# Performance work log

Hardware: AMD Instinct MI355X
Metric: run time of the kernel (lower is better)

## Reference

```python
import jax, jax.numpy as jnp
import numpy as np

NUM_PERSISTENT = 16
ALIBI_ALPHA = 1.0
START_I = 0
DILATION = 1
LN_EPS = 1e-5


def setup_inputs() -> dict:
    key = jax.random.key(0)
    ks = jax.random.split(key, 16)
    B, S, C, H = 8, 1024, 512, 8
    D = C // H
    P = NUM_PERSISTENT
    Kk = 3
    x = jax.random.normal(ks[0], (B, S, C), dtype=jnp.float32)
    mask = jnp.ones((B, 1, S, S), dtype=jnp.int32)
    sc = 0.02
    Wq = jax.random.normal(ks[1], (D, D), jnp.float32) * sc
    Wk = jax.random.normal(ks[2], (D, D), jnp.float32) * sc
    Wv = jax.random.normal(ks[3], (D, D), jnp.float32) * sc
    pk = jax.random.normal(ks[4], (P, H, D), jnp.float32) * sc
    pv = jax.random.normal(ks[5], (P, H, D), jnp.float32) * sc
    th_pre = jax.random.normal(ks[6], (H, H), jnp.float32) * (1.0 / np.sqrt(H))
    th_post = jax.random.normal(ks[7], (H, H), jnp.float32) * (1.0 / np.sqrt(H))
    fc_w = jax.random.normal(ks[8], (C, C), jnp.float32) * sc
    fc_b = jnp.zeros((C,), jnp.float32)
    conv1_w = jax.random.normal(ks[9], (C, C, Kk), jnp.float32) * 0.01
    conv1_b = jnp.zeros((C,), jnp.float32)
    conv2_w = jax.random.normal(ks[10], (C, C, Kk), jnp.float32) * 0.01
    conv2_b = jnp.zeros((C,), jnp.float32)
    ln_g = jnp.ones((C,), jnp.float32)
    ln_b = jnp.zeros((C,), jnp.float32)
    return dict(x=x, mask=mask, Wq=Wq, Wk=Wk, Wv=Wv, pk=pk, pv=pv,
                th_pre=th_pre, th_post=th_post, fc_w=fc_w, fc_b=fc_b,
                conv1_w=conv1_w, conv1_b=conv1_b, conv2_w=conv2_w,
                conv2_b=conv2_b, ln_g=ln_g, ln_b=ln_b)


def _causal_conv(x_nct, w_oik, b_o, dilation):
    # padding (k-1)*d on both sides + chomp right == pad left only
    k = w_oik.shape[-1]
    p = (k - 1) * dilation
    y = jax.lax.conv_general_dilated(
        x_nct, w_oik, window_strides=(1,), padding=[(p, 0)],
        rhs_dilation=(dilation,), dimension_numbers=("NCH", "OIH", "NCH"))
    return y + b_o[None, :, None]


def reference(x, mask, Wq, Wk, Wv, pk, pv, th_pre, th_post, fc_w, fc_b,
              conv1_w, conv1_b, conv2_w, conv2_b, ln_g, ln_b):
    N, S, C = x.shape
    H = th_pre.shape[0]
    D = C // H
    P = pk.shape[0]

    # ---- MultiHeadAttention (eval: dropout = identity) ----
    xh = x.reshape(N, S, H, D)
    q = jnp.einsum("nshd,ed->nshe", xh, Wq)
    k = jnp.einsum("nshd,ed->nshe", xh, Wk)
    v = jnp.einsum("nshd,ed->nshe", xh, Wv)
    # persistent memory tokens appended along key/value length
    k = jnp.concatenate([k, jnp.broadcast_to(pk[None], (N, P, H, D))], axis=1)
    v = jnp.concatenate([v, jnp.broadcast_to(pv[None], (N, P, H, D))], axis=1)

    energy = jnp.einsum("nqhd,nkhd->nhqk", q, k)  # (N,H,S,S+P)

    # ALiBi bias (symmetric |q-k|), zero over persistent keys
    slopes = 2.0 ** (-(ALIBI_ALPHA * (jnp.arange(1, H + 1, dtype=jnp.float32) + START_I)))
    t = jnp.arange(S, dtype=jnp.float32)
    dist = jnp.abs(t[:, None] - t[None, :])  # (S,S)
    bias = -dist[None, None] * slopes[None, :, None, None]  # (1,H,S,S)
    bias = jnp.pad(bias, ((0, 0), (0, 0), (0, 0), (0, P)))
    energy = energy + bias

    # pre-softmax talking heads (1x1 conv over head axis)
    energy = jnp.einsum("hg,ngqk->nhqk", th_pre, energy)

    ext_mask = jnp.pad(mask, ((0, 0), (0, 0), (0, 0), (0, P)), constant_values=1)
    energy = jnp.where(ext_mask == 0, jnp.float32(-1e4), energy)

    attn = jax.nn.softmax(energy / jnp.sqrt(jnp.float32(C)), axis=-1)
    attn = jnp.einsum("hg,ngqk->nhqk", th_post, attn)

    att_out = jnp.einsum("nhql,nlhd->nqhd", attn, v).reshape(N, S, C)
    att_out = att_out @ fc_w.T + fc_b

    x = x + att_out  # residual (dropout1 identity in eval)

    # ---- TemporalBlock (causal dilated convs, no SE since heads>0) ----
    xc = jnp.transpose(x, (0, 2, 1))  # (N,C,S)
    h = jax.nn.relu(_causal_conv(xc, conv1_w, conv1_b, DILATION))
    h = jax.nn.relu(_causal_conv(h, conv2_w, conv2_b, DILATION))
    out = jax.nn.relu(h + xc)  # downsample is None (in==out)

    # mask out invalid frames
    conv_mask = mask[:, 0, :, 0][:, None, :]  # (N,1,S)
    out = jnp.where(conv_mask == 0, 0.0, out)

    y = jnp.transpose(out, (0, 2, 1))  # (N,S,C)
    mu = jnp.mean(y, axis=-1, keepdims=True)
    var = jnp.mean(jnp.square(y - mu), axis=-1, keepdims=True)
    y = (y - mu) * jax.lax.rsqrt(var + LN_EPS) * ln_g + ln_b
    return y
```

## Files before the change

### kernel.cpp

```cpp
#include <hip/hip_runtime.h>
#include <hip/hip_bf16.h>

#define BN 8
#define SS 1024
#define CC 512
#define HH 8
#define DD 64
#define PP 16
#define KT 1040

typedef __hip_bfloat16 bf16;
typedef unsigned char uchar;
typedef unsigned short ushort;
typedef unsigned int uint;
typedef __attribute__((ext_vector_type(8))) short short8;
typedef __attribute__((ext_vector_type(4))) float f32x4;
typedef __attribute__((ext_vector_type(2))) float f32x2;

__device__ __forceinline__ short f2s(float v){ bf16 b = __float2bfloat16(v); return *(short*)&b; }
__device__ __forceinline__ float s2f(short s){ bf16 b; *(short*)&b = s; return __bfloat162float(b); }
__device__ __forceinline__ uchar f2q(float v){
    return (uchar)__builtin_amdgcn_cvt_pk_fp8_f32(v, v, 0, false);
}

#define MFMA16(a,b,c)  __builtin_amdgcn_mfma_f32_16x16x32_bf16(a,b,c,0,0,0)
#define MFMAF8(a,b,c)  __builtin_amdgcn_mfma_f32_16x16x32_fp8_fp8(a,b,c,0,0,0)

__global__ __launch_bounds__(256) void prep_kernel(
    const float* __restrict__ fc_w, const float* __restrict__ c1w,
    const float* __restrict__ c2w, const float* __restrict__ Wq,
    const float* __restrict__ Wk, const float* __restrict__ Wv,
    const float* __restrict__ th_post,
    const float* __restrict__ pk, const float* __restrict__ pv,
    short* __restrict__ Bfc, uchar* __restrict__ Bc1,
    uchar* __restrict__ Bc2, short* __restrict__ Bqkv,
    uchar* __restrict__ kf, uchar* __restrict__ vt)
{
    int i = blockIdx.x*256 + threadIdx.x;
    const int NFC = 512*512, NCV = 512*1536, NQ = 3*64*64, NP = BN*HH*PP*DD;
    if (i < NFC) {
        int c = i >> 9, r = i & 511;
        int g = r >> 6, d = r & 63;
        float s = 0.f;
        #pragma unroll
        for (int h = 0; h < 8; ++h)
            s += fc_w[(size_t)c*512 + h*64 + d] * th_post[h*8 + g];
        Bfc[i] = f2s(s);
        return;
    }
    i -= NFC;
    if (i < NCV) {
        int o = i/1536, r = i%1536, dk = r>>9, ci = r&511;
        Bc1[i] = f2q(c1w[(o*512+ci)*3+dk] * 16.f); return;
    }
    i -= NCV;
    if (i < NCV) {
        int o = i/1536, r = i%1536, dk = r>>9, ci = r&511;
        Bc2[i] = f2q(c2w[(o*512+ci)*3+dk] * 16.f); return;
    }
    i -= NCV;
    if (i < NQ) {
        int w = i >> 12, rest = i & 4095;
        const float* W = (w==0)?Wq:(w==1)?Wk:Wv;
        Bqkv[i] = f2s(W[((rest>>6)&63)*64 + (rest&63)]);
        return;
    }
    i -= NQ;
    if (i < NP) {
        int d = i & 63, p = (i >> 6) & 15, h = (i >> 10) & 7, n = i >> 13;
        size_t src = ((size_t)p*HH + h)*DD + d;
        kf[(((size_t)(n*HH+h))*KT + SS + p)*DD + d] = f2q(pk[src]);
        vt[(((size_t)(n*HH+h))*DD + d)*KT + SS + p] = f2q(pv[src]);
    }
}

__global__ __launch_bounds__(256) void qkv_mfma(
    const float* __restrict__ x, const short* __restrict__ Bqkv,
    uchar* __restrict__ qf, uchar* __restrict__ kf, uchar* __restrict__ vt)
{
    __shared__ short Xs[64*72];
    __shared__ short Ws[192*72];
    const int tid = threadIdx.x;
    const int lin = blockIdx.x;
    const int xcd = lin & 7, slot = lin >> 3;
    const int m0 = (xcd*16 + (slot & 15))*64;
    const int h = slot >> 4;
    const int wave = tid >> 6, lane = tid & 63;
    const int lr = lane & 15, lq = lane >> 4;

    for (int i = tid; i < 1024; i += 256) {
        int r = i >> 4, cg = (i & 15)*4;
        float4 v = *(const float4*)(x + (size_t)(m0+r)*CC + h*64 + cg);
        Xs[r*72+cg+0] = f2s(v.x); Xs[r*72+cg+1] = f2s(v.y);
        Xs[r*72+cg+2] = f2s(v.z); Xs[r*72+cg+3] = f2s(v.w);
    }
    for (int i = tid; i < 3072; i += 256) {
        int r = i >> 4, cg = (i & 15)*4;
        *(short4*)(Ws + r*72 + cg) = *(const short4*)(Bqkv + (size_t)r*64 + cg);
    }
    __syncthreads();

    f32x4 acc[12];
    #pragma unroll
    for (int nt = 0; nt < 12; ++nt) acc[nt] = {0.f,0.f,0.f,0.f};
    #pragma unroll
    for (int ks = 0; ks < 2; ++ks) {
        int ko = ks*32 + lq*8;
        short8 a = *(const short8*)(Xs + (wave*16 + lr)*72 + ko);
        #pragma unroll
        for (int nt = 0; nt < 12; ++nt) {
            short8 b = *(const short8*)(Ws + (nt*16 + lr)*72 + ko);
            acc[nt] = MFMA16(a, b, acc[nt]);
        }
    }
    #pragma unroll
    for (int nt = 0; nt < 12; ++nt) {
        int ep = nt*16 + lr;
        int w = ep >> 6, e = ep & 63;
        #pragma unroll
        for (int reg = 0; reg < 4; ++reg) {
            int m = m0 + wave*16 + lq*4 + reg;
            int n = m >> 10, s = m & 1023;
            float v = acc[nt][reg];
            if (w == 0)      qf[((size_t)(n*HH+h)*SS + s)*DD + e] = f2q(v);
            else if (w == 1) kf[((size_t)(n*HH+h)*KT + s)*DD + e] = f2q(v);
            else             vt[(((size_t)(n*HH+h))*DD + e)*KT + s] = f2q(v);
        }
    }
}

__device__ __forceinline__ void en_loadK(const uchar* __restrict__ kf,
    int nh, int kt, int tid, uint2* rk)
{
    #pragma unroll
    for (int j = 0; j < 2; ++j) {
        int i = tid + j*256;
        int r = i >> 3, c8 = (i & 7)*8;
        int kcol = kt*64 + r;
        uint2 v = {0u, 0u};
        if (kcol < KT)
            v = *(const uint2*)(kf + ((size_t)nh*KT + kcol)*DD + c8);
        rk[j] = v;
    }
}

__global__ __launch_bounds__(256) void energy_mfma8(
    const uchar* __restrict__ qf, const uchar* __restrict__ kf,
    uchar* __restrict__ E)
{
    __shared__ uchar Qs[64*72];
    __shared__ uchar Ks[64*72];
    const int tid = threadIdx.x;
    const int lin = blockIdx.x + 16*blockIdx.y;
    const int xcd = lin & 7, slot = lin >> 3;
    const int nh = xcd*8 + (slot & 7);
    const int mt = slot >> 3;
    const int wave = tid >> 6, lane = tid & 63;
    const int lr = lane & 15, lq = lane >> 4;
    const int n = nh >> 3, h = nh & 7;

    #pragma unroll
    for (int j = 0; j < 2; ++j) {
        int i = tid + j*256;
        int r = i >> 3, c8 = (i & 7)*8;
        *(uint2*)(Qs + r*72 + c8) =
            *(const uint2*)(qf + ((size_t)nh*SS + mt*64 + r)*DD + c8);
    }

    uint2 rk[2];
    en_loadK(kf, nh, 0, tid, rk);

    for (int kt = 0; kt < 17; ++kt) {
        if (kt) __syncthreads();
        #pragma unroll
        for (int j = 0; j < 2; ++j) {
            int i = tid + j*256;
            *(uint2*)(Ks + (i >> 3)*72 + (i & 7)*8) = rk[j];
        }
        __syncthreads();
        if (kt + 1 < 17) en_loadK(kf, nh, kt+1, tid, rk);

        f32x4 acc[4];
        #pragma unroll
        for (int nt = 0; nt < 4; ++nt) acc[nt] = {0.f,0.f,0.f,0.f};
        #pragma unroll
        for (int ks = 0; ks < 2; ++ks) {
            int ko = ks*32 + lq*8;
            long a = *(const long*)(Qs + (wave*16 + lr)*72 + ko);
            #pragma unroll
            for (int nt = 0; nt < 4; ++nt) {
                long b = *(const long*)(Ks + (nt*16 + lr)*72 + ko);
                acc[nt] = MFMAF8(a, b, acc[nt]);
            }
        }
        #pragma unroll
        for (int nt = 0; nt < 4; ++nt) {
            int kcol = kt*64 + nt*16 + lr;
            if (kcol >= KT) continue;
            #pragma unroll
            for (int reg = 0; reg < 4; ++reg) {
                int q = mt*64 + wave*16 + lq*4 + reg;
                E[(((size_t)(n*SS + q))*HH + h)*KT + kcol] = f2q(acc[nt][reg]);
            }
        }
    }
}

__global__ __launch_bounds__(256) void softmax_kernel(
    uchar* __restrict__ E, const int* __restrict__ mask,
    const float* __restrict__ th_pre)
{
    __shared__ float thp[64];
    __shared__ float wred[4][8];
    const int tid = threadIdx.x;
    const int wave = tid >> 6, lane = tid & 63;
    const int blk = blockIdx.x;
    const int n = blk >> 10, q = blk & 1023;
    const float invs = 0.044194173824159216f;
    const float l2e  = 1.4426950408889634f;
    if (tid < 64) thp[tid] = th_pre[tid]*(invs*l2e);
    __syncthreads();
    uchar* Eb = E + (size_t)blk*HH*KT;

    const float sl[8] = {0.5f,0.25f,0.125f,0.0625f,
                         0.03125f,0.015625f,0.0078125f,0.00390625f};
    const int* mrow = mask + (size_t)n*SS*SS + (size_t)q*SS;

    const int k0 = tid*4;
    const int4 mk = *(const int4*)(mrow + k0);
    f32x4 dist;
    dist.x = fabsf((float)(q - k0));
    dist.y = fabsf((float)(q - k0 - 1));
    dist.z = fabsf((float)(q - k0 - 2));
    dist.w = fabsf((float)(q - k0 - 3));

    f32x4 tp[8];
    float tl[8];
    float sm[8];
    #pragma unroll
    for (int g = 0; g < 8; ++g) { sm[g] = 0.f; tl[g] = 0.f; }

    {
        f32x4 a[8];
        #pragma unroll
        for (int g = 0; g < 8; ++g) {
            uint u = *(const uint*)(Eb + g*KT + k0);
            f32x2 lo = __builtin_amdgcn_cvt_pk_f32_fp8((int)u, false);
            f32x2 hi = __builtin_amdgcn_cvt_pk_f32_fp8((int)u, true);
            f32x4 r; r.x = lo.x; r.y = lo.y; r.z = hi.x; r.w = hi.y;
            a[g] = r - dist*sl[g];
        }
        #pragma unroll
        for (int h = 0; h < 8; ++h) {
            f32x4 t = {0.f,0.f,0.f,0.f};
            #pragma unroll
            for (int g = 0; g < 8; ++g)
                t += a[g] * thp[h*8 + g];
            f32x4 e;
            e.x = (mk.x == 0) ? 0.f : exp2f(t.x);
            e.y = (mk.y == 0) ? 0.f : exp2f(t.y);
            e.z = (mk.z == 0) ? 0.f : exp2f(t.z);
            e.w = (mk.w == 0) ? 0.f : exp2f(t.w);
            tp[h] = e;
            sm[h] += e.x + e.y + e.z + e.w;
        }
    }
    if (tid < 16) {
        const int k = 1024 + tid;
        float a[8];
        #pragma unroll
        for (int g = 0; g < 8; ++g) {
            f32x2 r = __builtin_amdgcn_cvt_pk_f32_fp8((int)Eb[g*KT + k], false);
            a[g] = r.x;
        }
        #pragma unroll
        for (int h = 0; h < 8; ++h) {
            float t = 0.f;
            #pragma unroll
            for (int g = 0; g < 8; ++g) t = fmaf(thp[h*8 + g], a[g], t);
            float e = exp2f(t);
            tl[h] = e;
            sm[h] += e;
        }
    }
    #pragma unroll
    for (int g = 0; g < 8; ++g) {
        #pragma unroll
        for (int off = 32; off > 0; off >>= 1)
            sm[g] += __shfl_xor(sm[g], off);
    }
    if (lane == 0) {
        #pragma unroll
        for (int g = 0; g < 8; ++g) wred[wave][g] = sm[g];
    }
    __syncthreads();
    float lred[8];
    #pragma unroll
    for (int g = 0; g < 8; ++g)
        lred[g] = 1.0f / (wred[0][g] + wred[1][g] + wred[2][g] + wred[3][g]);

    #pragma unroll
    for (int h = 0; h < 8; ++h) {
        f32x4 e = tp[h] * lred[h];
        int p = __builtin_amdgcn_cvt_pk_fp8_f32(e.x, e.y, 0, false);
        p = __builtin_amdgcn_cvt_pk_fp8_f32(e.z, e.w, p, true);
        *(uint*)(Eb + h*KT + k0) = (uint)p;
    }
    if (tid < 16) {
        const int k = 1024 + tid;
        #pragma unroll
        for (int g = 0; g < 8; ++g)
            Eb[g*KT + k] = f2q(tl[g] * lred[g]);
    }
}

__device__ __forceinline__ void pv_loadP(const uchar* __restrict__ E,
    int n, int h, int ql0, int kt, int tid, uint2* rp)
{
    #pragma unroll
    for (int j = 0; j < 2; ++j) {
        int i = tid + j*256;
        int r = i >> 3, cg = (i & 7)*8;
        int k = kt*64 + cg;
        uint2 v = {0u, 0u};
        if (k < KT)
            v = *(const uint2*)(E + (((size_t)(n*SS + ql0 + r))*HH + h)*KT + k);
        rp[j] = v;
    }
}
__device__ __forceinline__ void pv_loadV(const uchar* __restrict__ vt,
    int nh, int kt, int tid, uint2* rv)
{
    #pragma unroll
    for (int j = 0; j < 2; ++j) {
        int i = tid + j*256;
        int r = i >> 3, cg = (i & 7)*8;
        int k = kt*64 + cg;
        uint2 v = {0u, 0u};
        if (k < KT)
            v = *(const uint2*)(vt + ((size_t)nh*DD + r)*KT + k);
        rv[j] = v;
    }
}

__global__ __launch_bounds__(256) void pv_mfma(
    const uchar* __restrict__ E, const uchar* __restrict__ vt,
    short* __restrict__ AO)
{
    __shared__ uchar Ps[64*72];
    __shared__ uchar Vs[64*72];
    const int tid = threadIdx.x;
    const int lin = blockIdx.x + 16*blockIdx.y;
    const int xcd = lin & 7, slot = lin >> 3;
    const int nh = xcd*8 + (slot & 7);
    const int ql0 = (slot >> 3) * 64;
    const int n = nh >> 3, h = nh & 7;
    const int wave = tid >> 6, lane = tid & 63;
    const int lr = lane & 15, lq = lane >> 4;
    const int mq = (wave & 1)*32, nq = (wave >> 1)*32;

    uint2 rp[2], rv[2];
    pv_loadP(E, n, h, ql0, 0, tid, rp);
    pv_loadV(vt, nh, 0, tid, rv);

    f32x4 acc[2][2];
    #pragma unroll
    for (int i = 0; i < 2; ++i)
        #pragma unroll
        for (int j = 0; j < 2; ++j) acc[i][j] = {0.f,0.f,0.f,0.f};

    for (int kt = 0; kt < 17; ++kt) {
        if (kt) __syncthreads();
        #pragma unroll
        for (int j = 0; j < 2; ++j) {
            int i = tid + j*256;
            *(uint2*)(Ps + (i >> 3)*72 + (i & 7)*8) = rp[j];
        }
        #pragma unroll
        for (int j = 0; j < 2; ++j) {
            int i = tid + j*256;
            *(uint2*)(Vs + (i >> 3)*72 + (i & 7)*8) = rv[j];
        }
        __syncthreads();
        if (kt + 1 < 17) {
            pv_loadP(E, n, h, ql0, kt+1, tid, rp);
            pv_loadV(vt, nh, kt+1, tid, rv);
        }
        #pragma unroll
        for (int ks = 0; ks < 2; ++ks) {
            int ko = ks*32 + lq*8;
            long a0 = *(const long*)(Ps + (mq + lr)*72 + ko);
            long a1 = *(const long*)(Ps + (mq + 16 + lr)*72 + ko);
            long b0 = *(const long*)(Vs + (nq + lr)*72 + ko);
            long b1 = *(const long*)(Vs + (nq + 16 + lr)*72 + ko);
            acc[0][0] = MFMAF8(a0, b0, acc[0][0]);
            acc[0][1] = MFMAF8(a0, b1, acc[0][1]);
            acc[1][0] = MFMAF8(a1, b0, acc[1][0]);
            acc[1][1] = MFMAF8(a1, b1, acc[1][1]);
        }
    }
    #pragma unroll
    for (int mt = 0; mt < 2; ++mt)
        #pragma unroll
        for (int nt = 0; nt < 2; ++nt) {
            int d = nq + nt*16 + lr;
            #pragma unroll
            for (int reg = 0; reg < 4; ++reg) {
                int qg = ql0 + mq + mt*16 + lq*4 + reg;
                AO[((size_t)(n*SS) + qg)*CC + h*64 + d] = f2s(acc[mt][nt][reg]);
            }
        }
}

__device__ __forceinline__ void g_load4(const short* __restrict__ src,
    size_t rowstride, int row0, int col0, int tid, short4* r)
{
    #pragma unroll
    for (int j = 0; j < 4; ++j) {
        int i = tid + j*256;
        int rr = i >> 4, cg = (i & 15)*4;
        r[j] = *(const short4*)(src + (size_t)(row0 + rr)*rowstride + col0 + cg);
    }
}
__device__ __forceinline__ void lds_store4(short* __restrict__ dst,
    int tid, const short4* r)
{
    #pragma unroll
    for (int j = 0; j < 4; ++j) {
        int i = tid + j*256;
        *(short4*)(dst + (i >> 4)*72 + (i & 15)*4) = r[j];
    }
}

__global__ __launch_bounds__(256) void fc_mfma(
    const short* __restrict__ A, const short* __restrict__ Bt,
    const float* __restrict__ bias, const float* __restrict__ x,
    short* __restrict__ out, uchar* __restrict__ out8)
{
    __shared__ short As[64*72];
    __shared__ short Bs[64*72];
    const int tid = threadIdx.x;
    const int lin = blockIdx.x + 8*blockIdx.y;
    const int xcd = lin & 7, slot = lin >> 3;
    const int m0 = (xcd*16 + (slot & 15))*64;
    const int n0 = (slot >> 4)*64;
    const int wave = tid >> 6, lane = tid & 63;
    const int lr = lane & 15, lq = lane >> 4;

    short4 ra[4], rb[4];
    g_load4(A, CC, m0, 0, tid, ra);
    g_load4(Bt, CC, n0, 0, tid, rb);

    f32x4 acc[4];
    #pragma unroll
    for (int nt = 0; nt < 4; ++nt) acc[nt] = {0.f,0.f,0.f,0.f};

    for (int kt = 0; kt < CC; kt += 64) {
        if (kt) __syncthreads();
        lds_store4(As, tid, ra);
        lds_store4(Bs, tid, rb);
        __syncthreads();
        if (kt + 64 < CC) {
            g_load4(A, CC, m0, kt+64, tid, ra);
            g_load4(Bt, CC, n0, kt+64, tid, rb);
        }
        #pragma unroll
        for (int ks = 0; ks < 2; ++ks) {
            int ko = ks*32 + lq*8;
            short8 a = *(const short8*)(As + (wave*16 + lr)*72 + ko);
            #pragma unroll
            for (int nt = 0; nt < 4; ++nt) {
                short8 b = *(const short8*)(Bs + (nt*16 + lr)*72 + ko);
                acc[nt] = MFMA16(a, b, acc[nt]);
            }
        }
    }
    #pragma unroll
    for (int nt = 0; nt < 4; ++nt) {
        int nn = n0 + nt*16 + lr;
        #pragma unroll
        for (int reg = 0; reg < 4; ++reg) {
            int m = m0 + wave*16 + lq*4 + reg;
            float v = acc[nt][reg] + bias[nn] + x[(size_t)m*CC + nn];
            out[(size_t)m*CC + nn]  = f2s(v);
            out8[(size_t)m*CC + nn] = f2q(v);
        }
    }
}

__device__ __forceinline__ void conv_loadA8w(const uchar* __restrict__ A,
    int m0, int kt, int tid, uint2* ra)
{
    const int shift = (kt >> 9) - 2;
    const int ci0 = kt & 511;
    #pragma unroll
    for (int j = 0; j < 4; ++j) {
        int i = tid + j*256;
        int rr = i >> 4, c8 = (i & 15)*8;
        int m = m0 + rr;
        int s = m & (SS-1);
        uint2 v = {0u, 0u};
        if (s + shift >= 0)
            v = *(const uint2*)(A + (size_t)(m + shift)*CC + ci0 + c8);
        ra[j] = v;
    }
}
__device__ __forceinline__ void g_load8w(const uchar* __restrict__ src,
    size_t rowstride, int row0, int col0, int tid, uint2* r)
{
    #pragma unroll
    for (int j = 0; j < 4; ++j) {
        int i = tid + j*256;
        int rr = i >> 4, c8 = (i & 15)*8;
        r[j] = *(const uint2*)(src + (size_t)(row0 + rr)*rowstride + col0 + c8);
    }
}
__device__ __forceinline__ void lds_store8w(uchar* __restrict__ dst,
    int tid, const uint2* r)
{
    #pragma unroll
    for (int j = 0; j < 4; ++j) {
        int i = tid + j*256;
        *(uint2*)(dst + (i >> 4)*136 + (i & 15)*8) = r[j];
    }
}

__global__ __launch_bounds__(256) void conv_mfma8(
    const uchar* __restrict__ A, const uchar* __restrict__ Bt,
    const float* __restrict__ bias, uchar* __restrict__ out8,
    short* __restrict__ out16, int f8out)
{
    __shared__ uchar As[64*136];
    __shared__ uchar Bs[64*136];
    const int tid = threadIdx.x;
    const int lin = blockIdx.x + 8*blockIdx.y;
    const int xcd = lin & 7, slot = lin >> 3;
    const int m0 = (xcd*16 + (slot & 15))*64;
    const int n0 = (slot >> 4)*64;
    const int wave = tid >> 6, lane = tid & 63;
    const int lr = lane & 15, lq = lane >> 4;

    uint2 ra[4], rb[4];
    conv_loadA8w(A, m0, 0, tid, ra);
    g_load8w(Bt, 1536, n0, 0, tid, rb);

    f32x4 acc[4];
    #pragma unroll
    for (int nt = 0; nt < 4; ++nt) acc[nt] = {0.f,0.f,0.f,0.f};

    for (int kt = 0; kt < 1536; kt += 128) {
        if (kt) __syncthreads();
        lds_store8w(As, tid, ra);
        lds_store8w(Bs, tid, rb);
        __syncthreads();
        if (kt + 128 < 1536) {
            conv_loadA8w(A, m0, kt+128, tid, ra);
            g_load8w(Bt, 1536, n0, kt+128, tid, rb);
        }
        #pragma unroll
        for (int ks = 0; ks < 4; ++ks) {
            int ko = ks*32 + lq*8;
            long a = *(const long*)(As + (wave*16 + lr)*136 + ko);
            #pragma unroll
            for (int nt = 0; nt < 4; ++nt) {
                long b = *(const long*)(Bs + (nt*16 + lr)*136 + ko);
                acc[nt] = MFMAF8(a, b, acc[nt]);
            }
        }
    }
    #pragma unroll
    for (int nt = 0; nt < 4; ++nt) {
        int nn = n0 + nt*16 + lr;
        #pragma unroll
        for (int reg = 0; reg < 4; ++reg) {
            int m = m0 + wave*16 + lq*4 + reg;
            float v = fmaxf(acc[nt][reg]*0.0625f + bias[nn], 0.f);
            if (f8out) out8[(size_t)m*CC + nn]  = f2q(v);
            else       out16[(size_t)m*CC + nn] = f2s(v);
        }
    }
}

__global__ __launch_bounds__(256) void final_kernel(
    const short* __restrict__ c2, const short* __restrict__ xres,
    const int* __restrict__ mask, const float* __restrict__ g,
    const float* __restrict__ b, float* __restrict__ out)
{
    __shared__ float red[256];
    const int tid = threadIdx.x;
    const int m0 = blockIdx.x * 4;
    const int c0 = tid*2;
    const float2 gg = *(const float2*)(g + c0);
    const float2 bb = *(const float2*)(b + c0);

    for (int rr = 0; rr < 4; ++rr) {
        const int m = m0 + rr;
        const int n = m >> 10, s = m & 1023;
        const int mk = mask[(size_t)n*SS*SS + (size_t)s*SS];

        short2 ca = *(const short2*)(c2 + (size_t)m*CC + c0);
        short2 xa = *(const short2*)(xres + (size_t)m*CC + c0);
        float v0 = fmaxf(s2f(ca.x) + s2f(xa.x), 0.f);
        float v1 = fmaxf(s2f(ca.y) + s2f(xa.y), 0.f);
        if (mk == 0) { v0 = 0.f; v1 = 0.f; }

        red[tid] = v0 + v1;
        __syncthreads();
        for (int off = 128; off > 0; off >>= 1) {
            if (tid < off) red[tid] += red[tid + off];
            __syncthreads();
        }
        float mu = red[0] * (1.0f/512.0f);
        __syncthreads();
        float d0 = v0 - mu, d1 = v1 - mu;
        red[tid] = d0*d0 + d1*d1;
        __syncthreads();
        for (int off = 128; off > 0; off >>= 1) {
            if (tid < off) red[tid] += red[tid + off];
            __syncthreads();
        }
        float rstd = rsqrtf(red[0] * (1.0f/512.0f) + 1e-5f);
        float2 o;
        o.x = d0*rstd*gg.x + bb.x;
        o.y = d1*rstd*gg.y + bb.y;
        *(float2*)(out + (size_t)m*CC + c0) = o;
        __syncthreads();
    }
}

extern "C" void kernel_launch(void* const* d_in, const int* in_sizes, int n_in,
                              void* d_out, int out_size, void* d_ws, size_t ws_size,
                              hipStream_t stream)
{
    const float* x      = (const float*)d_in[0];
    const int*   mask   = (const int*)  d_in[1];
    const float* Wq     = (const float*)d_in[2];
    const float* Wk     = (const float*)d_in[3];
    const float* Wv     = (const float*)d_in[4];
    const float* pk     = (const float*)d_in[5];
    const float* pv     = (const float*)d_in[6];
    const float* th_pre = (const float*)d_in[7];
    const float* th_post= (const float*)d_in[8];
    const float* fc_w   = (const float*)d_in[9];
    const float* fc_b   = (const float*)d_in[10];
    const float* c1w    = (const float*)d_in[11];
    const float* c1b    = (const float*)d_in[12];
    const float* c2w    = (const float*)d_in[13];
    const float* c2b    = (const float*)d_in[14];
    const float* lng    = (const float*)d_in[15];
    const float* lnb    = (const float*)d_in[16];
    float* out = (float*)d_out;
    (void)in_sizes; (void)n_in; (void)out_size; (void)ws_size;

    char* ws = (char*)d_ws;
    const size_t SZ_Q  = (size_t)BN*HH*SS*DD;
    const size_t SZ_K  = (size_t)BN*HH*KT*DD;
    const size_t SZ_VT = (size_t)BN*HH*DD*KT;
    const size_t SZ_E  = (size_t)BN*SS*HH*KT;
    const size_t SZ_A  = (size_t)BN*SS*CC*2;
    const size_t SZ_A8 = (size_t)BN*SS*CC;

    uchar* qf  = (uchar*)(ws);
    uchar* kf  = (uchar*)(ws + SZ_Q);
    uchar* vt  = (uchar*)(ws + SZ_Q + SZ_K);
    uchar* E   = (uchar*)(ws + SZ_Q + SZ_K + SZ_VT);
    short* AO  = (short*)(ws + SZ_Q + SZ_K + SZ_VT + SZ_E);
    char*  wend = ws + SZ_Q + SZ_K + SZ_VT + SZ_E + SZ_A;
    short* Bfc = (short*)(wend);
    uchar* Bc1 = (uchar*)(wend + 512*512*2);
    uchar* Bc2 = (uchar*)(wend + 512*512*2 + 512*1536);
    short* Bqkv= (short*)(wend + 512*512*2 + 2*512*1536);
    uchar* xres8 = (uchar*)(wend + 512*512*2 + 2*512*1536 + 3*64*64*2);
    short* c2buf = (short*)(wend + 512*512*2 + 2*512*1536 + 3*64*64*2 + SZ_A8);
    short* xres = (short*)(ws);
    uchar* h18  = (uchar*)E;

    {
        int total = 512*512 + 2*512*1536 + 3*64*64 + BN*HH*PP*DD;
        prep_kernel<<<(total + 255)/256, 256, 0, stream>>>(
            fc_w, c1w, c2w, Wq, Wk, Wv, th_post, pk, pv,
            Bfc, Bc1, Bc2, Bqkv, kf, vt);
    }
    qkv_mfma<<<BN*SS/64*HH, 256, 0, stream>>>(x, Bqkv, qf, kf, vt);

    energy_mfma8<<<dim3(16, 64), 256, 0, stream>>>(qf, kf, E);
    softmax_kernel<<<BN*SS, 256, 0, stream>>>(E, mask, th_pre);
    pv_mfma<<<dim3(16, 64), 256, 0, stream>>>(E, vt, AO);

    fc_mfma<<<dim3(8, 128), 256, 0, stream>>>(AO, Bfc, fc_b, x, xres, xres8);
    conv_mfma8<<<dim3(8, 128), 256, 0, stream>>>(xres8, Bc1, c1b, h18, (short*)nullptr, 1);
    conv_mfma8<<<dim3(8, 128), 256, 0, stream>>>(h18, Bc2, c2b, (uchar*)nullptr, c2buf, 0);
    final_kernel<<<BN*SS/4, 256, 0, stream>>>(c2buf, xres, mask, lng, lnb, out);
}
```

Measured before the change: 284.6 us.

## Fuse softmax into PV kernel with deferred normalization

Removes the standalone softmax kernel. Each pv_fused block takes 16 queries across all 8 heads, turns the raw fp8 energies into exponentials in registers (with the th_pre head mix, ALiBi bias and mask), packs them to fp8 in LDS and feeds the MFMA PV product directly. The row-sum normalization is applied at output time, and a per-head analytic shift bound replaces a true row max. This avoids writing normalized probabilities back to E and reading them again. In exchange, each block reloads the full V tensor for its batch, and the grid is smaller (512 blocks), which lowers parallelism.

```diff
diff --git a/kernel.cpp b/kernel.cpp
--- a/kernel.cpp
+++ b/kernel.cpp
@@ -21,6 +21,9 @@
 __device__ __forceinline__ float s2f(short s){ bf16 b; *(short*)&b = s; return __bfloat162float(b); }
 __device__ __forceinline__ uchar f2q(float v){
     return (uchar)__builtin_amdgcn_cvt_pk_fp8_f32(v, v, 0, false);
+}
+__device__ __forceinline__ float rfl(float x){
+    return __int_as_float(__builtin_amdgcn_readfirstlane(__float_as_int(x)));
 }
 
 #define MFMA16(a,b,c)  __builtin_amdgcn_mfma_f32_16x16x32_bf16(a,b,c,0,0,0)
@@ -206,210 +209,184 @@
     }
 }
 
-__global__ __launch_bounds__(256) void softmax_kernel(
-    uchar* __restrict__ E, const int* __restrict__ mask,
-    const float* __restrict__ th_pre)
-{
-    __shared__ float thp[64];
-    __shared__ float wred[4][8];
-    const int tid = threadIdx.x;
-    const int wave = tid >> 6, lane = tid & 63;
-    const int blk = blockIdx.x;
-    const int n = blk >> 10, q = blk & 1023;
-    const float invs = 0.044194173824159216f;
-    const float l2e  = 1.4426950408889634f;
-    if (tid < 64) thp[tid] = th_pre[tid]*(invs*l2e);
-    __syncthreads();
-    uchar* Eb = E + (size_t)blk*HH*KT;
-
-    const float sl[8] = {0.5f,0.25f,0.125f,0.0625f,
-                         0.03125f,0.015625f,0.0078125f,0.00390625f};
-    const int* mrow = mask + (size_t)n*SS*SS + (size_t)q*SS;
-
-    const int k0 = tid*4;
-    const int4 mk = *(const int4*)(mrow + k0);
-    f32x4 dist;
-    dist.x = fabsf((float)(q - k0));
-    dist.y = fabsf((float)(q - k0 - 1));
-    dist.z = fabsf((float)(q - k0 - 2));
-    dist.w = fabsf((float)(q - k0 - 3));
-
-    f32x4 tp[8];
-    float tl[8];
-    float sm[8];
-    #pragma unroll
-    for (int g = 0; g < 8; ++g) { sm[g] = 0.f; tl[g] = 0.f; }
-
-    {
-        f32x4 a[8];
-        #pragma unroll
-        for (int g = 0; g < 8; ++g) {
-            uint u = *(const uint*)(Eb + g*KT + k0);
-            f32x2 lo = __builtin_amdgcn_cvt_pk_f32_fp8((int)u, false);
-            f32x2 hi = __builtin_amdgcn_cvt_pk_f32_fp8((int)u, true);
-            f32x4 r; r.x = lo.x; r.y = lo.y; r.z = hi.x; r.w = hi.y;
-            a[g] = r - dist*sl[g];
-        }
-        #pragma unroll
-        for (int h = 0; h < 8; ++h) {
-            f32x4 t = {0.f,0.f,0.f,0.f};
-            #pragma unroll
-            for (int g = 0; g < 8; ++g)
-                t += a[g] * thp[h*8 + g];
-            f32x4 e;
-            e.x = (mk.x == 0) ? 0.f : exp2f(t.x);
-            e.y = (mk.y == 0) ? 0.f : exp2f(t.y);
-            e.z = (mk.z == 0) ? 0.f : exp2f(t.z);
-            e.w = (mk.w == 0) ? 0.f : exp2f(t.w);
-            tp[h] = e;
-            sm[h] += e.x + e.y + e.z + e.w;
-        }
-    }
-    if (tid < 16) {
-        const int k = 1024 + tid;
-        float a[8];
-        #pragma unroll
-        for (int g = 0; g < 8; ++g) {
-            f32x2 r = __builtin_amdgcn_cvt_pk_f32_fp8((int)Eb[g*KT + k], false);
-            a[g] = r.x;
-        }
-        #pragma unroll
-        for (int h = 0; h < 8; ++h) {
-            float t = 0.f;
-            #pragma unroll
-            for (int g = 0; g < 8; ++g) t = fmaf(thp[h*8 + g], a[g], t);
-            float e = exp2f(t);
-            tl[h] = e;
-            sm[h] += e;
-        }
-    }
-    #pragma unroll
-    for (int g = 0; g < 8; ++g) {
-        #pragma unroll
-        for (int off = 32; off > 0; off >>= 1)
-            sm[g] += __shfl_xor(sm[g], off);
-    }
-    if (lane == 0) {
-        #pragma unroll
-        for (int g = 0; g < 8; ++g) wred[wave][g] = sm[g];
-    }
-    __syncthreads();
-    float lred[8];
-    #pragma unroll
-    for (int g = 0; g < 8; ++g)
-        lred[g] = 1.0f / (wred[0][g] + wred[1][g] + wred[2][g] + wred[3][g]);
-
-    #pragma unroll
-    for (int h = 0; h < 8; ++h) {
-        f32x4 e = tp[h] * lred[h];
-        int p = __builtin_amdgcn_cvt_pk_fp8_f32(e.x, e.y, 0, false);
-        p = __builtin_amdgcn_cvt_pk_fp8_f32(e.z, e.w, p, true);
-        *(uint*)(Eb + h*KT + k0) = (uint)p;
-    }
-    if (tid < 16) {
-        const int k = 1024 + tid;
+__device__ __forceinline__ void pvf_loadE(const uchar* __restrict__ Eb,
+    int kt, int k4, uint* rE)
+{
+    int kb = kt*64 + k4;
+    if (kb < KT) {
         #pragma unroll
         for (int g = 0; g < 8; ++g)
-            Eb[g*KT + k] = f2q(tl[g] * lred[g]);
-    }
-}
-
-__device__ __forceinline__ void pv_loadP(const uchar* __restrict__ E,
-    int n, int h, int ql0, int kt, int tid, uint2* rp)
-{
-    #pragma unroll
-    for (int j = 0; j < 2; ++j) {
-        int i = tid + j*256;
-        int r = i >> 3, cg = (i & 7)*8;
-        int k = kt*64 + cg;
-        uint2 v = {0u, 0u};
-        if (k < KT)
-            v = *(const uint2*)(E + (((size_t)(n*SS + ql0 + r))*HH + h)*KT + k);
-        rp[j] = v;
-    }
-}
-__device__ __forceinline__ void pv_loadV(const uchar* __restrict__ vt,
-    int nh, int kt, int tid, uint2* rv)
-{
-    #pragma unroll
-    for (int j = 0; j < 2; ++j) {
-        int i = tid + j*256;
-        int r = i >> 3, cg = (i & 7)*8;
-        int k = kt*64 + cg;
-        uint2 v = {0u, 0u};
-        if (k < KT)
-            v = *(const uint2*)(vt + ((size_t)nh*DD + r)*KT + k);
-        rv[j] = v;
-    }
-}
-
-__global__ __launch_bounds__(256) void pv_mfma(
+            rE[g] = *(const uint*)(Eb + (size_t)g*KT + kb);
+    } else {
+        #pragma unroll
+        for (int g = 0; g < 8; ++g) rE[g] = 0u;
+    }
+}
+__device__ __forceinline__ void pvf_loadV(const uchar* __restrict__ vtb,
+    int kt, int tid, uint4* rv)
+{
+    #pragma unroll
+    for (int j = 0; j < 8; ++j) {
+        int i = tid + j*256;
+        rv[j] = *(const uint4*)(vtb + (size_t)(i >> 2)*KT + kt*64 + (i & 3)*16);
+    }
+}
+
+__global__ __launch_bounds__(256, 2) void pv_fused(
     const uchar* __restrict__ E, const uchar* __restrict__ vt,
+    const int* __restrict__ mask, const float* __restrict__ th_pre,
     short* __restrict__ AO)
 {
-    __shared__ uchar Ps[64*72];
-    __shared__ uchar Vs[64*72];
-    const int tid = threadIdx.x;
-    const int lin = blockIdx.x + 16*blockIdx.y;
-    const int xcd = lin & 7, slot = lin >> 3;
-    const int nh = xcd*8 + (slot & 7);
-    const int ql0 = (slot >> 3) * 64;
-    const int n = nh >> 3, h = nh & 7;
+    __shared__ uchar Ps[8*16*72];
+    __shared__ uchar Vs[8*64*72];
+    __shared__ float Sred[16][8];
+    const int tid  = threadIdx.x;
+    const int n    = blockIdx.x;
+    const int ql0  = blockIdx.y * 16;
     const int wave = tid >> 6, lane = tid & 63;
     const int lr = lane & 15, lq = lane >> 4;
-    const int mq = (wave & 1)*32, nq = (wave >> 1)*32;
-
-    uint2 rp[2], rv[2];
-    pv_loadP(E, n, h, ql0, 0, tid, rp);
-    pv_loadV(vt, nh, 0, tid, rv);
-
-    f32x4 acc[2][2];
+    const int q_l = tid >> 4, kq = tid & 15, k4 = kq*4;
+    const int q = ql0 + q_l;
+
+    const float sc = 0.044194173824159216f * 1.4426950408889634f;
+    float thp_s[64], slmix_s[8], shift_s[8];
+    {
+        const float slv[8] = {0.5f,0.25f,0.125f,0.0625f,
+                              0.03125f,0.015625f,0.0078125f,0.00390625f};
+        const float maxd = (float)((q > SS-1-q) ? q : (SS-1-q));
+        #pragma unroll
+        for (int h = 0; h < 8; ++h) {
+            float sm = 0.f;
+            #pragma unroll
+            for (int g = 0; g < 8; ++g) {
+                float v = rfl(th_pre[h*8+g] * sc);
+                thp_s[h*8+g] = v;
+                sm += v * slv[g];
+            }
+            slmix_s[h] = rfl(sm);
+            shift_s[h] = fmaxf(0.f, -slmix_s[h] * maxd);
+        }
+    }
+
+    const uchar* Eb  = E  + ((size_t)(n*SS + q))*HH*KT;
+    const uchar* vtb = vt + (size_t)n*HH*DD*KT;
+    const int*  mrow = mask + (size_t)n*SS*SS + (size_t)q*SS;
+
+    uint  rE[8]; uint4 rv[8]; int4 rm;
+    pvf_loadE(Eb, 0, k4, rE);
+    pvf_loadV(vtb, 0, tid, rv);
+    rm = *(const int4*)(mrow + k4);
+
+    f32x4 sums4[8];
+    #pragma unroll
+    for (int h = 0; h < 8; ++h) sums4[h] = {0.f,0.f,0.f,0.f};
+    f32x4 acc[2][4];
     #pragma unroll
     for (int i = 0; i < 2; ++i)
         #pragma unroll
-        for (int j = 0; j < 2; ++j) acc[i][j] = {0.f,0.f,0.f,0.f};
+        for (int j = 0; j < 4; ++j) acc[i][j] = {0.f,0.f,0.f,0.f};
 
     for (int kt = 0; kt < 17; ++kt) {
-        if (kt) __syncthreads();
-        #pragma unroll
-        for (int j = 0; j < 2; ++j) {
+        uint pb[8];
+        {
+            f32x4 a[8];
+            #pragma unroll
+            for (int g = 0; g < 8; ++g) {
+                f32x2 lo = __builtin_amdgcn_cvt_pk_f32_fp8((int)rE[g], false);
+                f32x2 hi = __builtin_amdgcn_cvt_pk_f32_fp8((int)rE[g], true);
+                f32x4 r; r.x = lo.x; r.y = lo.y; r.z = hi.x; r.w = hi.y;
+                a[g] = r;
+            }
+            const bool body = (kt < 16);
+            const bool pvalid = (kt*64 + k4) < KT;
+            float kb = (float)(kt*64 + k4), qv = (float)q;
+            f32x4 dist;
+            dist.x = fabsf(qv - kb);       dist.y = fabsf(qv - kb - 1.f);
+            dist.z = fabsf(qv - kb - 2.f); dist.w = fabsf(qv - kb - 3.f);
+            #pragma unroll
+            for (int h = 0; h < 8; ++h) {
+                f32x4 t = {0.f,0.f,0.f,0.f};
+                #pragma unroll
+                for (int g = 0; g < 8; ++g) t += a[g] * thp_s[h*8+g];
+                const float shf = shift_s[h];
+                f32x4 e;
+                if (body) {
+                    t -= dist * slmix_s[h];
+                    e.x = (rm.x == 0) ? 0.f : exp2f(t.x - shf);
+                    e.y = (rm.y == 0) ? 0.f : exp2f(t.y - shf);
+                    e.z = (rm.z == 0) ? 0.f : exp2f(t.z - shf);
+                    e.w = (rm.w == 0) ? 0.f : exp2f(t.w - shf);
+                } else if (pvalid) {
+                    e.x = exp2f(t.x - shf); e.y = exp2f(t.y - shf);
+                    e.z = exp2f(t.z - shf); e.w = exp2f(t.w - shf);
+                } else {
+                    e = {0.f,0.f,0.f,0.f};
+                }
+                sums4[h] += e;
+                int p0 = __builtin_amdgcn_cvt_pk_fp8_f32(e.x, e.y, 0, false);
+                p0 = __builtin_amdgcn_cvt_pk_fp8_f32(e.z, e.w, p0, true);
+                pb[h] = (uint)p0;
+            }
+        }
+        __syncthreads();
+        #pragma unroll
+        for (int h = 0; h < 8; ++h)
+            *(uint*)(Ps + h*1152 + q_l*72 + k4) = pb[h];
+        #pragma unroll
+        for (int j = 0; j < 8; ++j) {
             int i = tid + j*256;
-            *(uint2*)(Ps + (i >> 3)*72 + (i & 7)*8) = rp[j];
-        }
-        #pragma unroll
-        for (int j = 0; j < 2; ++j) {
-            int i = tid + j*256;
-            *(uint2*)(Vs + (i >> 3)*72 + (i & 7)*8) = rv[j];
+            uchar* d = Vs + (i >> 2)*72 + (i & 3)*16;
+            uint2 lo; lo.x = rv[j].x; lo.y = rv[j].y;
+            uint2 hi; hi.x = rv[j].z; hi.y = rv[j].w;
+            *(uint2*)(d) = lo; *(uint2*)(d + 8) = hi;
         }
         __syncthreads();
         if (kt + 1 < 17) {
-            pv_loadP(E, n, h, ql0, kt+1, tid, rp);
-            pv_loadV(vt, nh, kt+1, tid, rv);
-        }
-        #pragma unroll
-        for (int ks = 0; ks < 2; ++ks) {
-            int ko = ks*32 + lq*8;
-            long a0 = *(const long*)(Ps + (mq + lr)*72 + ko);
-            long a1 = *(const long*)(Ps + (mq + 16 + lr)*72 + ko);
-            long b0 = *(const long*)(Vs + (nq + lr)*72 + ko);
-            long b1 = *(const long*)(Vs + (nq + 16 + lr)*72 + ko);
-            acc[0][0] = MFMAF8(a0, b0, acc[0][0]);
-            acc[0][1] = MFMAF8(a0, b1, acc[0][1]);
-            acc[1][0] = MFMAF8(a1, b0, acc[1][0]);
-            acc[1][1] = MFMAF8(a1, b1, acc[1][1]);
-        }
-    }
-    #pragma unroll
-    for (int mt = 0; mt < 2; ++mt)
-        #pragma unroll
-        for (int nt = 0; nt < 2; ++nt) {
-            int d = nq + nt*16 + lr;
-            #pragma unroll
-            for (int reg = 0; reg < 4; ++reg) {
-                int qg = ql0 + mq + mt*16 + lq*4 + reg;
-                AO[((size_t)(n*SS) + qg)*CC + h*64 + d] = f2s(acc[mt][nt][reg]);
-            }
-        }
+            pvf_loadE(Eb, kt+1, k4, rE);
+            pvf_loadV(vtb, kt+1, tid, rv);
+            if (kt + 1 < 16) rm = *(const int4*)(mrow + (kt+1)*64 + k4);
+        }
+        #pragma unroll
+        for (int h2 = 0; h2 < 2; ++h2) {
+            const uchar* Ph = Ps + (wave*2 + h2)*1152;
+            const uchar* Vh = Vs + (wave*2 + h2)*4608;
+            #pragma unroll
+            for (int ks = 0; ks < 2; ++ks) {
+                int ko = ks*32 + lq*8;
+                long av = *(const long*)(Ph + lr*72 + ko);
+                #pragma unroll
+                for (int nt = 0; nt < 4; ++nt) {
+                    long bv = *(const long*)(Vh + (nt*16 + lr)*72 + ko);
+                    acc[h2][nt] = MFMAF8(av, bv, acc[h2][nt]);
+                }
+            }
+        }
+    }
+
+    #pragma unroll
+    for (int h = 0; h < 8; ++h) {
+        float s = sums4[h].x + sums4[h].y + sums4[h].z + sums4[h].w;
+        s += __shfl_xor(s, 1); s += __shfl_xor(s, 2);
+        s += __shfl_xor(s, 4); s += __shfl_xor(s, 8);
+        if (kq == 0) Sred[q_l][h] = 1.0f / s;
+    }
+    __syncthreads();
+
+    #pragma unroll
+    for (int h2 = 0; h2 < 2; ++h2) {
+        int h = wave*2 + h2;
+        #pragma unroll
+        for (int reg = 0; reg < 4; ++reg) {
+            float inv = Sred[lq*4 + reg][h];
+            int qg = ql0 + lq*4 + reg;
+            #pragma unroll
+            for (int nt = 0; nt < 4; ++nt) {
+                int d = nt*16 + lr;
+                AO[((size_t)(n*SS) + qg)*CC + h*64 + d] =
+                    f2s(acc[h2][nt][reg] * inv);
+            }
+        }
+    }
 }
 
 __device__ __forceinline__ void g_load4(const short* __restrict__ src,
@@ -684,8 +661,7 @@
     qkv_mfma<<<BN*SS/64*HH, 256, 0, stream>>>(x, Bqkv, qf, kf, vt);
 
     energy_mfma8<<<dim3(16, 64), 256, 0, stream>>>(qf, kf, E);
-    softmax_kernel<<<BN*SS, 256, 0, stream>>>(E, mask, th_pre);
-    pv_mfma<<<dim3(16, 64), 256, 0, stream>>>(E, vt, AO);
+    pv_fused<<<dim3(8, 64), 256, 0, stream>>>(E, vt, mask, th_pre, AO);
 
     fc_mfma<<<dim3(8, 128), 256, 0, stream>>>(AO, Bfc, fc_b, x, xres, xres8);
     conv_mfma8<<<dim3(8, 128), 256, 0, stream>>>(xres8, Bc1, c1b, h18, (short*)nullptr, 1);
```

After: 780.9 us. 2.74x slower.
